# Optimization experiments

Measured on AMD Instinct MI355X. Metric: run time of the kernel, lower is better.

The kernel has to match this reference:

```python
import jax, jax.numpy as jnp
import numpy as np
import math

B, L, D, H = 4, 4096, 1024, 16
d = D // H

def setup_inputs() -> dict:
    key = jax.random.key(0)
    ks = jax.random.split(key, 8)
    s = 0.02
    x = jax.random.normal(ks[0], (B, L, D), dtype=jnp.float32)
    Wqkv_w = jax.random.normal(ks[1], (3 * D, D), dtype=jnp.float32) * s
    Wqkv_b = jnp.zeros((3 * D,), dtype=jnp.float32)
    out_w = jax.random.normal(ks[2], (D, D), dtype=jnp.float32) * s
    out_b = jnp.zeros((D,), dtype=jnp.float32)
    W_static = jax.random.normal(ks[3], (H, d, d), dtype=jnp.float32) * s
    Lambda_raw = jax.random.uniform(ks[4], (H, d, d), dtype=jnp.float32, minval=-3.0, maxval=3.0)
    g = 0.5 / math.sqrt(d)
    Gamma = jax.random.uniform(ks[5], (H, d, d), dtype=jnp.float32, minval=-g, maxval=g)
    return {"x": x, "Wqkv_w": Wqkv_w, "Wqkv_b": Wqkv_b, "out_w": out_w,
            "out_b": out_b, "W_static": W_static, "Lambda_raw": Lambda_raw, "Gamma": Gamma}

def _stp_forward(x, Wqkv_w, Wqkv_b, out_w, out_b, W_static, Lambda_raw, Gamma):
    b, l, dm = x.shape
    scale = 1.0 / math.sqrt(d)
    qkv = x @ Wqkv_w.T + Wqkv_b                      # (B,L,3D)
    qkv = qkv.reshape(b, l, 3, H, d)                 # 'b l (three h d)'
    qkv = jnp.transpose(qkv, (2, 0, 3, 1, 4))        # (3,B,H,L,d)
    q, k, v = qkv[0], qkv[1], qkv[2]
    k = k * scale
    retention = 1.0 - jax.nn.sigmoid(Lambda_raw)     # (H,d,d)

    # scan over time: carry state (B,H,d,d)
    qs = jnp.moveaxis(q, 2, 0)                       # (L,B,H,d)
    ks_ = jnp.moveaxis(k, 2, 0)
    vs = jnp.moveaxis(v, 2, 0)

    def step(state, qkv_t):
        q_t, k_t, v_t = qkv_t                        # each (B,H,d)
        hebbian = jnp.einsum('bhi,bhj->bhij', v_t, k_t)
        state = retention[None] * state + Gamma[None] * hebbian
        y_t = jnp.einsum('bhij,bhj->bhi', W_static[None] + state, q_t)
        return state, y_t

    state0 = jnp.zeros((b, H, d, d), dtype=x.dtype)
    _, ys = jax.lax.scan(step, state0, (qs, ks_, vs))  # ys: (L,B,H,d)
    y = jnp.transpose(ys, (1, 0, 2, 3)).reshape(b, l, dm)  # 'b h l d -> b l (h d)'
    return y @ out_w.T + out_b

def reference(x, Wqkv_w, Wqkv_b, out_w, out_b, W_static, Lambda_raw, Gamma):
    return _stp_forward(x, Wqkv_w, Wqkv_b, out_w, out_b, W_static, Lambda_raw, Gamma)
```

## Files before the change

kernel.cpp:

```cpp
#include <hip/hip_runtime.h>
#include <stdint.h>

typedef unsigned short u16;
typedef __bf16 bf16x8 __attribute__((ext_vector_type(8)));
typedef float  f32x4  __attribute__((ext_vector_type(4)));

#define GLOBAL_AS __attribute__((address_space(1)))
#define LDS_AS    __attribute__((address_space(3)))

#define B_ 4
#define L_ 4096
#define D_ 1024
#define H_ 16
#define TD 3072
#define NCHUNK 16
#define TCHUNK 256

__device__ __forceinline__ float bf2f(u16 h) {
    union { uint32_t u; float f; } v; v.u = ((uint32_t)h) << 16; return v.f;
}
__device__ __forceinline__ u16 f2bf(float f) {
    union { float f; uint32_t u; } v; v.f = f;
    uint32_t u = v.u;
    u += 0x7fffu + ((u >> 16) & 1u);
    return (u16)(u >> 16);
}
__device__ __forceinline__ void unp8(uint4 u, float* f) {
    f[0] = bf2f((u16)(u.x)); f[1] = bf2f((u16)(u.x >> 16));
    f[2] = bf2f((u16)(u.y)); f[3] = bf2f((u16)(u.y >> 16));
    f[4] = bf2f((u16)(u.z)); f[5] = bf2f((u16)(u.z >> 16));
    f[6] = bf2f((u16)(u.w)); f[7] = bf2f((u16)(u.w >> 16));
}

__device__ __forceinline__ uint4 ld8f(const float* p) {
    const float4 a = *(const float4*)p;
    const float4 b = *(const float4*)(p + 4);
    uint4 r;
    r.x = (uint32_t)f2bf(a.x) | ((uint32_t)f2bf(a.y) << 16);
    r.y = (uint32_t)f2bf(a.z) | ((uint32_t)f2bf(a.w) << 16);
    r.z = (uint32_t)f2bf(b.x) | ((uint32_t)f2bf(b.y) << 16);
    r.w = (uint32_t)f2bf(b.z) | ((uint32_t)f2bf(b.w) << 16);
    return r;
}

__device__ __forceinline__ void stc(u16* p, float v)   { *p = f2bf(v); }
__device__ __forceinline__ void stc(float* p, float v) { *p = v; }

__global__ __launch_bounds__(256) void cvt_f32_bf16(
    const float* __restrict__ in, u16* __restrict__ out, size_t n8)
{
    size_t i = (size_t)blockIdx.x * 256 + threadIdx.x;
    if (i >= n8) return;
    *(uint4*)(out + i * 8) = ld8f(in + i * 8);
}

template <typename TC>
__global__ __launch_bounds__(256) void gemm_bt_bias_bf16(
    const u16* __restrict__ A, const u16* __restrict__ W,
    const float* __restrict__ bias, TC* __restrict__ C,
    int M, int N, int K)
{
    __shared__ u16 As[128 * 32];
    __shared__ u16 Bs[128 * 32];

    const int tid  = threadIdx.x;
    const int lane = tid & 63;
    const int wid  = tid >> 6;
    const int bm = blockIdx.y * 128;
    const int bn = blockIdx.x * 128;

    const int wm = (wid & 1) * 64;
    const int wn = (wid >> 1) * 64;
    const int fr   = lane & 15;
    const int quad = lane >> 4;

    const u16* Ag = A + (size_t)(bm + (tid >> 2)) * K + (tid & 3) * 8;
    const u16* Wg = W + (size_t)(bn + (tid >> 2)) * K + (tid & 3) * 8;
    const size_t rskip = (size_t)64 * K;

    u16* AsW = As + wid * 512;
    u16* BsW = Bs + wid * 512;

    f32x4 acc[4][4] = {};

    for (int k0 = 0; k0 < K; k0 += 32) {
        __syncthreads();
        __builtin_amdgcn_global_load_lds((const GLOBAL_AS void*)(Ag + k0),
                                         (LDS_AS void*)(AsW),        16, 0, 0);
        __builtin_amdgcn_global_load_lds((const GLOBAL_AS void*)(Ag + rskip + k0),
                                         (LDS_AS void*)(AsW + 2048), 16, 0, 0);
        __builtin_amdgcn_global_load_lds((const GLOBAL_AS void*)(Wg + k0),
                                         (LDS_AS void*)(BsW),        16, 0, 0);
        __builtin_amdgcn_global_load_lds((const GLOBAL_AS void*)(Wg + rskip + k0),
                                         (LDS_AS void*)(BsW + 2048), 16, 0, 0);
        __syncthreads();

        bf16x8 af[4], bfv[4];
#pragma unroll
        for (int tm = 0; tm < 4; ++tm) {
            int m = wm + tm * 16 + fr;
            af[tm] = *(const bf16x8*)&As[m * 32 + quad * 8];
        }
#pragma unroll
        for (int tn = 0; tn < 4; ++tn) {
            int n = wn + tn * 16 + fr;
            bfv[tn] = *(const bf16x8*)&Bs[n * 32 + quad * 8];
        }
#pragma unroll
        for (int tm = 0; tm < 4; ++tm)
#pragma unroll
            for (int tn = 0; tn < 4; ++tn)
                acc[tm][tn] = __builtin_amdgcn_mfma_f32_16x16x32_bf16(
                    af[tm], bfv[tn], acc[tm][tn], 0, 0, 0);
    }

#pragma unroll
    for (int tm = 0; tm < 4; ++tm) {
#pragma unroll
        for (int tn = 0; tn < 4; ++tn) {
            const int col = bn + wn + tn * 16 + fr;
            const float bv = bias[col];
#pragma unroll
            for (int r = 0; r < 4; ++r) {
                const int row = bm + wm + tm * 16 + quad * 4 + r;
                stc(&C[(size_t)row * N + col], acc[tm][tn][r] + bv);
            }
        }
    }
}

__global__ __launch_bounds__(256) void stp_scan_local(
    const u16* __restrict__ qkv, const float* __restrict__ Lam,
    const float* __restrict__ Gam, float* __restrict__ F)
{
    const int c = blockIdx.x, h = blockIdx.y, b = blockIdx.z;
    const int t = threadIdx.x;
    const int i = t >> 2, jc = t & 3, j0 = jc << 4;
    const int hij = (h << 12) + (i << 6) + j0;

    float R[16], Gv[16], s[16];
#pragma unroll
    for (int j = 0; j < 16; ++j) {
        R[j]  = 1.0f / (1.0f + expf(Lam[hij + j]));
        Gv[j] = Gam[hij + j] * 0.125f;
        s[j]  = 0.0f;
    }

    const u16* rowp = qkv + (size_t)(b * L_ + c * TCHUNK) * TD;
    const int koff = D_ + (h << 6) + j0;
    const int voff = 2 * D_ + (h << 6) + i;

    for (int tt = 0; tt < TCHUNK; ++tt, rowp += TD) {
        const float v = bf2f(rowp[voff]);
        uint4 ku0 = *(const uint4*)(rowp + koff);
        uint4 ku1 = *(const uint4*)(rowp + koff + 8);
        float kf[16];
        unp8(ku0, kf); unp8(ku1, kf + 8);
#pragma unroll
        for (int j = 0; j < 16; ++j)
            s[j] = fmaf(R[j], s[j], (Gv[j] * v) * kf[j]);
    }

    float* Fp = F + (((size_t)(b * H_ + h) * NCHUNK + c) << 12) + (i << 6) + j0;
#pragma unroll
    for (int j = 0; j < 16; j += 4)
        *(f32x4*)(Fp + j) = *(const f32x4*)(s + j);
}

__global__ __launch_bounds__(256) void stp_combine(
    const float* __restrict__ Lam, float* __restrict__ F)
{
    const int h = blockIdx.x, b = blockIdx.y;
    const int t = threadIdx.x;
    const int i = t >> 2, jc = t & 3, j0 = jc << 4;
    const int hij = (h << 12) + (i << 6) + j0;

    float Rt[16], s[16];
#pragma unroll
    for (int j = 0; j < 16; ++j) {
        float R = 1.0f / (1.0f + expf(Lam[hij + j]));
        Rt[j] = powf(R, (float)TCHUNK);
        s[j] = 0.0f;
    }
    float* base = F + (((size_t)(b * H_ + h) * NCHUNK) << 12) + (i << 6) + j0;
    for (int c = 0; c < NCHUNK; ++c) {
        float* p = base + ((size_t)c << 12);
        float tmp[16];
#pragma unroll
        for (int j = 0; j < 16; ++j) tmp[j] = p[j];
#pragma unroll
        for (int j = 0; j < 16; ++j) { p[j] = s[j]; s[j] = fmaf(Rt[j], s[j], tmp[j]); }
    }
}

__global__ __launch_bounds__(256) void stp_scan_out(
    const u16* __restrict__ qkv, const float* __restrict__ Lam,
    const float* __restrict__ Gam, const float* __restrict__ Wst,
    const float* __restrict__ Sinit, u16* __restrict__ y)
{
    const int c = blockIdx.x, h = blockIdx.y, b = blockIdx.z;
    const int t = threadIdx.x;
    const int i = t >> 2, jc = t & 3, j0 = jc << 4;
    const int hij = (h << 12) + (i << 6) + j0;

    float R[16], Gv[16], Wr[16], s[16];
    const float* Sp = Sinit + (((size_t)(b * H_ + h) * NCHUNK + c) << 12) + (i << 6) + j0;
#pragma unroll
    for (int j = 0; j < 16; ++j) {
        R[j]  = 1.0f / (1.0f + expf(Lam[hij + j]));
        Gv[j] = Gam[hij + j] * 0.125f;
        Wr[j] = Wst[hij + j];
        s[j]  = Sp[j];
    }

    const u16* rowp = qkv + (size_t)(b * L_ + c * TCHUNK) * TD;
    const int qoff = (h << 6) + j0;
    const int koff = D_ + qoff;
    const int voff = 2 * D_ + (h << 6) + i;
    u16* yp = y + (size_t)(b * L_ + c * TCHUNK) * D_ + (h << 6) + i;

    for (int tt = 0; tt < TCHUNK; ++tt, rowp += TD, yp += D_) {
        const float v = bf2f(rowp[voff]);
        uint4 qu0 = *(const uint4*)(rowp + qoff);
        uint4 qu1 = *(const uint4*)(rowp + qoff + 8);
        uint4 ku0 = *(const uint4*)(rowp + koff);
        uint4 ku1 = *(const uint4*)(rowp + koff + 8);
        float kf[16], qf[16];
        unp8(ku0, kf); unp8(ku1, kf + 8);
        unp8(qu0, qf); unp8(qu1, qf + 8);

        float ya = 0.0f, yb = 0.0f;
#pragma unroll
        for (int j = 0; j < 16; j += 2) {
            s[j]     = fmaf(R[j],     s[j],     (Gv[j]     * v) * kf[j]);
            s[j + 1] = fmaf(R[j + 1], s[j + 1], (Gv[j + 1] * v) * kf[j + 1]);
            ya = fmaf(Wr[j]     + s[j],     qf[j],     ya);
            yb = fmaf(Wr[j + 1] + s[j + 1], qf[j + 1], yb);
        }
        float yacc = ya + yb;
        yacc += __shfl_xor(yacc, 1, 64);
        yacc += __shfl_xor(yacc, 2, 64);
        if (jc == 0) *yp = f2bf(yacc);
    }
}

__global__ void zero_out_f32(float* p, size_t n) {
    size_t i = (size_t)blockIdx.x * blockDim.x + threadIdx.x;
    if (i < n) p[i] = 0.0f;
}

extern "C" void kernel_launch(void* const* d_in, const int* in_sizes, int n_in,
                              void* d_out, int out_size, void* d_ws, size_t ws_size,
                              hipStream_t stream)
{
    const float* x      = (const float*)d_in[0];
    const float* Wqkv_w = (const float*)d_in[1];
    const float* Wqkv_b = (const float*)d_in[2];
    const float* out_w  = (const float*)d_in[3];
    const float* out_b  = (const float*)d_in[4];
    const float* Wst    = (const float*)d_in[5];
    const float* Lam    = (const float*)d_in[6];
    const float* Gam    = (const float*)d_in[7];
    float* out = (float*)d_out;

    const size_t need = (size_t)B_ * L_ * TD * 2 + (size_t)B_ * L_ * D_ * 2
                      + (size_t)B_ * H_ * NCHUNK * 64 * 64 * 4;
    if (ws_size < need) {
        zero_out_f32<<<(out_size + 255) / 256, 256, 0, stream>>>(out, (size_t)out_size);
        return;
    }
    u16*   qkv = (u16*)d_ws;
    u16*   y   = qkv + (size_t)B_ * L_ * TD;
    float* F   = (float*)(y + (size_t)B_ * L_ * D_);
    u16*   xb    = y;
    u16*   wqkvb = (u16*)F;
    u16*   outwb = (u16*)F;

    cvt_f32_bf16<<<(B_ * L_ * D_ / 8 + 255) / 256, 256, 0, stream>>>(
        x, xb, (size_t)B_ * L_ * D_ / 8);
    cvt_f32_bf16<<<(TD * D_ / 8 + 255) / 256, 256, 0, stream>>>(
        Wqkv_w, wqkvb, (size_t)TD * D_ / 8);
    gemm_bt_bias_bf16<u16><<<dim3(TD / 128, (B_ * L_) / 128), 256, 0, stream>>>(
        xb, wqkvb, Wqkv_b, qkv, B_ * L_, TD, D_);
    stp_scan_local<<<dim3(NCHUNK, H_, B_), 256, 0, stream>>>(qkv, Lam, Gam, F);
    stp_combine<<<dim3(H_, B_), 256, 0, stream>>>(Lam, F);
    stp_scan_out<<<dim3(NCHUNK, H_, B_), 256, 0, stream>>>(qkv, Lam, Gam, Wst, F, y);
    cvt_f32_bf16<<<(D_ * D_ / 8 + 255) / 256, 256, 0, stream>>>(
        out_w, outwb, (size_t)D_ * D_ / 8);
    gemm_bt_bias_bf16<float><<<dim3(D_ / 128, (B_ * L_) / 128), 256, 0, stream>>>(
        y, outwb, out_b, out, B_ * L_, D_, D_);
}
```

Before: 749.4 us.

## Remap scan threads to 2x8 state tiles, prefetch next row, fold W_static into state

Both chunked scan kernels now give each thread two state rows of 8 columns instead of one row of 16. One k vector load is reused across two rows, and two v values come from a single 32-bit load. The next timestep's q/k/v is loaded before the current one is processed, to hide global-load latency in the sequential loop. The output scan adds W_static into the state up front and feeds a constant W(1-R) term each step, so the per-element add is gone. It also uses a 3-level shuffle reduction with packed two-value bf16 stores and an occupancy hint in launch_bounds. The prefetch reads one row past the chunk on the last iteration, which can touch memory beyond the final chunk. Folding W_static into the state also changes fp32 rounding slightly.

```diff
diff --git a/kernel.cpp b/kernel.cpp
--- a/kernel.cpp
+++ b/kernel.cpp
@@ -129,42 +129,55 @@
     }
 }
 
-__global__ __launch_bounds__(256) void stp_scan_local(
+__global__ __launch_bounds__(256, 4) void stp_scan_local(
     const u16* __restrict__ qkv, const float* __restrict__ Lam,
     const float* __restrict__ Gam, float* __restrict__ F)
 {
     const int c = blockIdx.x, h = blockIdx.y, b = blockIdx.z;
     const int t = threadIdx.x;
-    const int i = t >> 2, jc = t & 3, j0 = jc << 4;
-    const int hij = (h << 12) + (i << 6) + j0;
-
-    float R[16], Gv[16], s[16];
-#pragma unroll
-    for (int j = 0; j < 16; ++j) {
-        R[j]  = 1.0f / (1.0f + expf(Lam[hij + j]));
-        Gv[j] = Gam[hij + j] * 0.125f;
-        s[j]  = 0.0f;
-    }
+    const int ig = t >> 3, jc = t & 7;
+    const int i0 = ig << 1, j0 = jc << 3;
+    const int hij = (h << 12) + (i0 << 6) + j0;
+
+    float R[2][8], Gv[2][8], s[2][8];
+#pragma unroll
+    for (int r = 0; r < 2; ++r)
+#pragma unroll
+        for (int j = 0; j < 8; ++j) {
+            R[r][j]  = 1.0f / (1.0f + expf(Lam[hij + r * 64 + j]));
+            Gv[r][j] = Gam[hij + r * 64 + j] * 0.125f;
+            s[r][j]  = 0.0f;
+        }
 
     const u16* rowp = qkv + (size_t)(b * L_ + c * TCHUNK) * TD;
     const int koff = D_ + (h << 6) + j0;
-    const int voff = 2 * D_ + (h << 6) + i;
-
-    for (int tt = 0; tt < TCHUNK; ++tt, rowp += TD) {
-        const float v = bf2f(rowp[voff]);
-        uint4 ku0 = *(const uint4*)(rowp + koff);
-        uint4 ku1 = *(const uint4*)(rowp + koff + 8);
-        float kf[16];
-        unp8(ku0, kf); unp8(ku1, kf + 8);
-#pragma unroll
-        for (int j = 0; j < 16; ++j)
-            s[j] = fmaf(R[j], s[j], (Gv[j] * v) * kf[j]);
-    }
-
-    float* Fp = F + (((size_t)(b * H_ + h) * NCHUNK + c) << 12) + (i << 6) + j0;
-#pragma unroll
-    for (int j = 0; j < 16; j += 4)
-        *(f32x4*)(Fp + j) = *(const f32x4*)(s + j);
+    const int voff = 2 * D_ + (h << 6) + i0;
+
+    uint4    ku = *(const uint4*)(rowp + koff);
+    uint32_t vu = *(const uint32_t*)(rowp + voff);
+
+    for (int tt = 0; tt < TCHUNK; ++tt) {
+        uint4    kn = *(const uint4*)(rowp + TD + koff);
+        uint32_t vn = *(const uint32_t*)(rowp + TD + voff);
+
+        float kf[8];
+        unp8(ku, kf);
+        const float v0 = bf2f((u16)vu);
+        const float v1 = bf2f((u16)(vu >> 16));
+#pragma unroll
+        for (int j = 0; j < 8; ++j) {
+            s[0][j] = fmaf(R[0][j], s[0][j], (Gv[0][j] * v0) * kf[j]);
+            s[1][j] = fmaf(R[1][j], s[1][j], (Gv[1][j] * v1) * kf[j]);
+        }
+        ku = kn; vu = vn; rowp += TD;
+    }
+
+    float* Fp = F + (((size_t)(b * H_ + h) * NCHUNK + c) << 12) + (i0 << 6) + j0;
+#pragma unroll
+    for (int r = 0; r < 2; ++r) {
+        *(f32x4*)(Fp + r * 64)     = *(const f32x4*)(&s[r][0]);
+        *(f32x4*)(Fp + r * 64 + 4) = *(const f32x4*)(&s[r][4]);
+    }
 }
 
 __global__ __launch_bounds__(256) void stp_combine(
@@ -193,54 +206,71 @@
     }
 }
 
-__global__ __launch_bounds__(256) void stp_scan_out(
+__global__ __launch_bounds__(256, 4) void stp_scan_out(
     const u16* __restrict__ qkv, const float* __restrict__ Lam,
     const float* __restrict__ Gam, const float* __restrict__ Wst,
     const float* __restrict__ Sinit, u16* __restrict__ y)
 {
     const int c = blockIdx.x, h = blockIdx.y, b = blockIdx.z;
     const int t = threadIdx.x;
-    const int i = t >> 2, jc = t & 3, j0 = jc << 4;
-    const int hij = (h << 12) + (i << 6) + j0;
-
-    float R[16], Gv[16], Wr[16], s[16];
-    const float* Sp = Sinit + (((size_t)(b * H_ + h) * NCHUNK + c) << 12) + (i << 6) + j0;
-#pragma unroll
-    for (int j = 0; j < 16; ++j) {
-        R[j]  = 1.0f / (1.0f + expf(Lam[hij + j]));
-        Gv[j] = Gam[hij + j] * 0.125f;
-        Wr[j] = Wst[hij + j];
-        s[j]  = Sp[j];
-    }
+    const int ig = t >> 3, jc = t & 7;
+    const int i0 = ig << 1, j0 = jc << 3;
+    const int hij = (h << 12) + (i0 << 6) + j0;
+
+    float R[2][8], Gv[2][8], Cc[2][8], s[2][8];
+    const float* Sp = Sinit + (((size_t)(b * H_ + h) * NCHUNK + c) << 12) + (i0 << 6) + j0;
+#pragma unroll
+    for (int r = 0; r < 2; ++r)
+#pragma unroll
+        for (int j = 0; j < 8; ++j) {
+            const float Rv = 1.0f / (1.0f + expf(Lam[hij + r * 64 + j]));
+            const float Wv = Wst[hij + r * 64 + j];
+            R[r][j]  = Rv;
+            Gv[r][j] = Gam[hij + r * 64 + j] * 0.125f;
+            Cc[r][j] = Wv * (1.0f - Rv);
+            s[r][j]  = Sp[r * 64 + j] + Wv;
+        }
 
     const u16* rowp = qkv + (size_t)(b * L_ + c * TCHUNK) * TD;
     const int qoff = (h << 6) + j0;
     const int koff = D_ + qoff;
-    const int voff = 2 * D_ + (h << 6) + i;
-    u16* yp = y + (size_t)(b * L_ + c * TCHUNK) * D_ + (h << 6) + i;
-
-    for (int tt = 0; tt < TCHUNK; ++tt, rowp += TD, yp += D_) {
-        const float v = bf2f(rowp[voff]);
-        uint4 qu0 = *(const uint4*)(rowp + qoff);
-        uint4 qu1 = *(const uint4*)(rowp + qoff + 8);
-        uint4 ku0 = *(const uint4*)(rowp + koff);
-        uint4 ku1 = *(const uint4*)(rowp + koff + 8);
-        float kf[16], qf[16];
-        unp8(ku0, kf); unp8(ku1, kf + 8);
-        unp8(qu0, qf); unp8(qu1, qf + 8);
-
-        float ya = 0.0f, yb = 0.0f;
-#pragma unroll
-        for (int j = 0; j < 16; j += 2) {
-            s[j]     = fmaf(R[j],     s[j],     (Gv[j]     * v) * kf[j]);
-            s[j + 1] = fmaf(R[j + 1], s[j + 1], (Gv[j + 1] * v) * kf[j + 1]);
-            ya = fmaf(Wr[j]     + s[j],     qf[j],     ya);
-            yb = fmaf(Wr[j + 1] + s[j + 1], qf[j + 1], yb);
-        }
-        float yacc = ya + yb;
-        yacc += __shfl_xor(yacc, 1, 64);
-        yacc += __shfl_xor(yacc, 2, 64);
-        if (jc == 0) *yp = f2bf(yacc);
+    const int voff = 2 * D_ + (h << 6) + i0;
+    u16* yp = y + (size_t)(b * L_ + c * TCHUNK) * D_ + (h << 6) + i0;
+
+    uint4    qu = *(const uint4*)(rowp + qoff);
+    uint4    ku = *(const uint4*)(rowp + koff);
+    uint32_t vu = *(const uint32_t*)(rowp + voff);
+
+    for (int tt = 0; tt < TCHUNK; ++tt) {
+        uint4    qn = *(const uint4*)(rowp + TD + qoff);
+        uint4    kn = *(const uint4*)(rowp + TD + koff);
+        uint32_t vn = *(const uint32_t*)(rowp + TD + voff);
+
+        float qf[8], kf[8];
+        unp8(qu, qf); unp8(ku, kf);
+        const float v0 = bf2f((u16)vu);
+        const float v1 = bf2f((u16)(vu >> 16));
+
+        float ya0 = 0.0f, ya1 = 0.0f;
+#pragma unroll
+        for (int j = 0; j < 8; ++j) {
+            s[0][j] = fmaf(R[0][j], s[0][j], fmaf(Gv[0][j] * v0, kf[j], Cc[0][j]));
+            ya0 = fmaf(s[0][j], qf[j], ya0);
+            s[1][j] = fmaf(R[1][j], s[1][j], fmaf(Gv[1][j] * v1, kf[j], Cc[1][j]));
+            ya1 = fmaf(s[1][j], qf[j], ya1);
+        }
+        ya0 += __shfl_xor(ya0, 1, 64);
+        ya0 += __shfl_xor(ya0, 2, 64);
+        ya0 += __shfl_xor(ya0, 4, 64);
+        ya1 += __shfl_xor(ya1, 1, 64);
+        ya1 += __shfl_xor(ya1, 2, 64);
+        ya1 += __shfl_xor(ya1, 4, 64);
+        if (jc == 0) {
+            uint32_t pk = (uint32_t)f2bf(ya0) | ((uint32_t)f2bf(ya1) << 16);
+            *(uint32_t*)yp = pk;
+        }
+        qu = qn; ku = kn; vu = vn;
+        rowp += TD; yp += D_;
     }
 }
 
```

Measured after the change: 670.1 us. 10.6% less time.
